# Kernel tuning notes

Hardware: AMD Instinct MI355X
Metric: run time of the kernel (lower is better)

Reference implementation:

```python
import jax, jax.numpy as jnp
import numpy as np

N, E = 100000, 1600000
NFEAT, NHID, NOUT, NHEADS = 512, 64, 64, 8
ALPHA = 0.2  # LeakyReLU negative slope


def setup_inputs() -> dict:
    key = jax.random.key(0)
    ks = jax.random.split(key, 12)
    feat = jax.random.normal(ks[0], (N, NFEAT), dtype=jnp.float32)
    edge_index = jax.random.randint(ks[1], (2, E), 0, N, dtype=jnp.int32)
    s = 0.05
    return {
        "feat": feat,
        "edge_index": edge_index,
        "fW_w": jax.random.normal(ks[2], (NHEADS, NHID, NFEAT), dtype=jnp.float32) * s,
        "fW_b": jnp.zeros((NHEADS, NHID), dtype=jnp.float32),
        "a_src": jax.random.normal(ks[3], (NHEADS, NHID), dtype=jnp.float32) * s,
        "a_dest": jax.random.normal(ks[4], (NHEADS, NHID), dtype=jnp.float32) * s,
        "W0": jax.random.normal(ks[5], (NHEADS, NHID, NFEAT), dtype=jnp.float32) * s,
        "b0": jnp.zeros((NHEADS, NHID), dtype=jnp.float32),
        "W1": jax.random.normal(ks[6], (NHEADS, NHID, NHEADS * NHID), dtype=jnp.float32) * s,
        "b1": jnp.zeros((NHEADS, NHID), dtype=jnp.float32),
        "lin_w": jax.random.normal(ks[7], (NOUT, NHEADS * NHID), dtype=jnp.float32) * s,
        "lin_b": jnp.zeros((NOUT,), dtype=jnp.float32),
    }


def reference(feat, edge_index, fW_w, fW_b, a_src, a_dest, W0, b0, W1, b1, lin_w, lin_b):
    n = feat.shape[0]
    row, col = edge_index[0], edge_index[1]

    # feature attention (all heads at once): h = fW(feat)  [N,H,D]
    h = jnp.einsum('nf,hdf->nhd', feat, fW_w) + fW_b
    f1 = jnp.einsum('nhd,hd->nh', h, a_src)   # [N,H]
    f2 = jnp.einsum('nhd,hd->nh', h, a_dest)  # [N,H]
    e = f1[row] + f2[col]                     # [E,H]
    e = jnp.where(e > 0, e, ALPHA * e)        # LeakyReLU
    # sparse softmax over each row's neighborhood (dim=1 of adj)
    m = jax.ops.segment_max(e, row, num_segments=n)    # [N,H]
    ex = jnp.exp(e - m[row])
    denom = jax.ops.segment_sum(ex, row, num_segments=n)
    attn = ex / denom[row]                    # [E,H]

    def spmm(vals, xw):  # vals [E], xw [N,D] -> [N,D]
        return jax.ops.segment_sum(vals[:, None] * xw[col], row, num_segments=n)

    x = feat
    for Wl, bl in ((W0, b0), (W1, b1)):
        outs = []
        for hidx in range(NHEADS):
            xw = x @ Wl[hidx].T + bl[hidx]           # [N,NHID]
            outs.append(jax.nn.elu(spmm(attn[:, hidx], xw)))
        x = jnp.concatenate(outs, axis=1)            # [N, H*NHID]

    return x @ lin_w.T + lin_b
```

## Files before the change

kernel.cpp:

```cpp
#include <hip/hip_runtime.h>
#include <hip/hip_bf16.h>
#include <math.h>

#define NFEAT 512
#define NHID  64
#define NHEADS 8
#define HD    512
#define NOUT  64

typedef _Float16 half8 __attribute__((ext_vector_type(8)));
typedef _Float16 half4 __attribute__((ext_vector_type(4)));
typedef float floatx4 __attribute__((ext_vector_type(4)));

__global__ void g_k(const float* __restrict__ fW_w, const float* __restrict__ fW_b,
                    const float* __restrict__ a_src, const float* __restrict__ a_dest,
                    float* __restrict__ G, float* __restrict__ C16)
{
    int idx = blockIdx.x * blockDim.x + threadIdx.x;
    if (idx < 16 * 512) {
        int r = idx >> 9;
        int f = idx & 511;
        int h = r & 7;
        const float* a = (r < 8) ? a_src : a_dest;
        float s = 0.f;
        #pragma unroll 8
        for (int d = 0; d < 64; ++d)
            s = fmaf(fW_w[(size_t)(h * 64 + d) * 512 + f], a[h * 64 + d], s);
        G[(size_t)r * 512 + f] = s;
    } else if (idx < 16 * 512 + 16) {
        int r = idx - 16 * 512;
        int h = r & 7;
        const float* a = (r < 8) ? a_src : a_dest;
        float s = 0.f;
        for (int d = 0; d < 64; ++d)
            s = fmaf(fW_b[h * 64 + d], a[h * 64 + d], s);
        C16[r] = s;
    }
}

#define FB_BM 128
#define FB_BK 64
__global__ __launch_bounds__(256) void f1f2_k(const float* __restrict__ feat,
    const float* __restrict__ G, const float* __restrict__ C16,
    float* __restrict__ f1, float* __restrict__ f2,
    _Float16* __restrict__ featH, int M)
{
    __shared__ float As[FB_BK][FB_BM + 4];
    __shared__ float Gs[16][FB_BK + 1];
    int tid = threadIdx.x;
    int tx = tid & 15;
    int ty = tid >> 4;
    int m0 = blockIdx.x * FB_BM;
    float acc[8] = {0.f, 0.f, 0.f, 0.f, 0.f, 0.f, 0.f, 0.f};

    for (int k0 = 0; k0 < NFEAT; k0 += FB_BK) {
        __syncthreads();
        #pragma unroll
        for (int j = 0; j < 8; ++j) {
            int fid = tid + 256 * j;
            int ml = fid >> 4;
            int k4 = fid & 15;
            float4 v = make_float4(0.f, 0.f, 0.f, 0.f);
            int gm = m0 + ml;
            if (gm < M) {
                v = *(const float4*)(feat + (size_t)gm * NFEAT + k0 + k4 * 4);
                half4 hv;
                hv[0] = (_Float16)v.x; hv[1] = (_Float16)v.y;
                hv[2] = (_Float16)v.z; hv[3] = (_Float16)v.w;
                *(half4*)(featH + (size_t)gm * NFEAT + k0 + k4 * 4) = hv;
            }
            As[k4 * 4 + 0][ml] = v.x;
            As[k4 * 4 + 1][ml] = v.y;
            As[k4 * 4 + 2][ml] = v.z;
            As[k4 * 4 + 3][ml] = v.w;
        }
        {
            int gr = tid >> 4;
            int k4 = tid & 15;
            float4 v = *(const float4*)(G + (size_t)gr * 512 + k0 + k4 * 4);
            Gs[gr][k4 * 4 + 0] = v.x;
            Gs[gr][k4 * 4 + 1] = v.y;
            Gs[gr][k4 * 4 + 2] = v.z;
            Gs[gr][k4 * 4 + 3] = v.w;
        }
        __syncthreads();
        #pragma unroll 16
        for (int kk = 0; kk < FB_BK; ++kk) {
            float g = Gs[tx][kk];
            #pragma unroll
            for (int i = 0; i < 8; ++i)
                acc[i] = fmaf(As[kk][ty + 16 * i], g, acc[i]);
        }
    }
    float c = C16[tx];
    #pragma unroll
    for (int i = 0; i < 8; ++i) {
        int gm = m0 + ty + 16 * i;
        if (gm < M) {
            float v = acc[i] + c;
            if (tx < 8) f1[(size_t)gm * 8 + tx] = v;
            else        f2[(size_t)gm * 8 + (tx - 8)] = v;
        }
    }
}

__global__ void zero_k(int* __restrict__ deg, int* __restrict__ fill, int n)
{
    int i = blockIdx.x * blockDim.x + threadIdx.x;
    if (i < n) { deg[i] = 0; fill[i] = 0; }
}

__global__ void count_k(const int* __restrict__ ei, int* __restrict__ deg, int E)
{
    int e = blockIdx.x * blockDim.x + threadIdx.x;
    if (e < E) atomicAdd(&deg[ei[e]], 1);
}

__global__ __launch_bounds__(1024) void bscan_k(const int* __restrict__ deg,
    int* __restrict__ row_ptr, int* __restrict__ bsum, int n)
{
    __shared__ int sh[1024];
    int tid = threadIdx.x;
    int i = blockIdx.x * 1024 + tid;
    int x = (i < n) ? deg[i] : 0;
    sh[tid] = x;
    __syncthreads();
    for (int off = 1; off < 1024; off <<= 1) {
        int v = (tid >= off) ? sh[tid - off] : 0;
        __syncthreads();
        sh[tid] += v;
        __syncthreads();
    }
    if (i < n) row_ptr[i] = sh[tid] - x;
    if (tid == 1023) bsum[blockIdx.x] = sh[1023];
}

__global__ void sscan_k(int* __restrict__ bsum, int nb)
{
    if (blockIdx.x == 0 && threadIdx.x == 0) {
        int run = 0;
        for (int b = 0; b < nb; ++b) { int t = bsum[b]; bsum[b] = run; run += t; }
    }
}

__global__ void addoff_k(int* __restrict__ row_ptr, const int* __restrict__ bsum,
                         int n, int Etot)
{
    int i = blockIdx.x * blockDim.x + threadIdx.x;
    if (i < n) row_ptr[i] += bsum[i >> 10];
    if (i == 0) row_ptr[n] = Etot;
}

__global__ void fill_k(const int* __restrict__ ei, const int* __restrict__ row_ptr,
                       int* __restrict__ fill, int* __restrict__ col_s, int E)
{
    int e = blockIdx.x * blockDim.x + threadIdx.x;
    if (e >= E) return;
    int r = ei[e];
    int c = ei[E + e];
    int o = atomicAdd(&fill[r], 1);
    col_s[row_ptr[r] + o] = c;
}

__global__ void attn_k(const int* __restrict__ row_ptr, const int* __restrict__ col_s,
                       const float* __restrict__ f1, const float* __restrict__ f2,
                       float* __restrict__ attn_s, float* __restrict__ inv_den,
                       int n_rows)
{
    int n = blockIdx.x * blockDim.x + threadIdx.x;
    if (n >= n_rows) return;
    int s = row_ptr[n], epos = row_ptr[n + 1];
    float4 fa = *(const float4*)(f1 + (size_t)n * 8);
    float4 fb = *(const float4*)(f1 + (size_t)n * 8 + 4);
    float F1[8] = {fa.x, fa.y, fa.z, fa.w, fb.x, fb.y, fb.z, fb.w};
    float den[8] = {0.f, 0.f, 0.f, 0.f, 0.f, 0.f, 0.f, 0.f};
    for (int p = s; p < epos; ++p) {
        int c = col_s[p];
        float4 ga = *(const float4*)(f2 + (size_t)c * 8);
        float4 gb = *(const float4*)(f2 + (size_t)c * 8 + 4);
        float F2[8] = {ga.x, ga.y, ga.z, ga.w, gb.x, gb.y, gb.z, gb.w};
        float ex[8];
        #pragma unroll
        for (int h = 0; h < 8; ++h) {
            float t = F1[h] + F2[h];
            t = (t > 0.f) ? t : 0.2f * t;
            ex[h] = expf(t);
            den[h] += ex[h];
        }
        float4* ap = (float4*)(attn_s + (size_t)p * 8);
        ap[0] = make_float4(ex[0], ex[1], ex[2], ex[3]);
        ap[1] = make_float4(ex[4], ex[5], ex[6], ex[7]);
    }
    float4* ip = (float4*)(inv_den + (size_t)n * 8);
    float iv[8];
    #pragma unroll
    for (int h = 0; h < 8; ++h) iv[h] = (den[h] > 0.f) ? 1.f / den[h] : 0.f;
    ip[0] = make_float4(iv[0], iv[1], iv[2], iv[3]);
    ip[1] = make_float4(iv[4], iv[5], iv[6], iv[7]);
}

__global__ void cvt_f16_k(const float* __restrict__ in, _Float16* __restrict__ out,
                          size_t n)
{
    size_t i = ((size_t)blockIdx.x * blockDim.x + threadIdx.x) * 8;
    if (i >= n) return;
    float4 a = *(const float4*)(in + i);
    float4 b = *(const float4*)(in + i + 4);
    half8 h;
    h[0] = (_Float16)a.x; h[1] = (_Float16)a.y; h[2] = (_Float16)a.z; h[3] = (_Float16)a.w;
    h[4] = (_Float16)b.x; h[5] = (_Float16)b.y; h[6] = (_Float16)b.z; h[7] = (_Float16)b.w;
    *(half8*)(out + i) = h;
}

#define TM 128
#define TN 128
#define TK 32
__global__ __launch_bounds__(256) void gemm_f16_mfma(
    const _Float16* __restrict__ A,
    const _Float16* __restrict__ B,
    const float* __restrict__ bias,
    _Float16* __restrict__ C,
    int M, int N, int K)
{
    __shared__ _Float16 smem_h[TM * TK + TN * TK];
    _Float16* Ash = smem_h;
    _Float16* Bsh = smem_h + TM * TK;
    int tid = threadIdx.x;
    int wave = tid >> 6;
    int lane = tid & 63;
    int m0 = blockIdx.x * TM;
    int n0 = blockIdx.y * TN;
    int wm = (wave & 1) * 64;
    int wn = (wave >> 1) * 64;

    floatx4 acc[4][4] = {};

    int fm = lane & 15;
    int q  = lane >> 4;

    for (int k0 = 0; k0 < K; k0 += TK) {
        __syncthreads();
        #pragma unroll
        for (int t = 0; t < 2; ++t) {
            int r = wave * 16 + t * 64;
            int gr = m0 + r + (lane >> 2);
            if (gr > M - 1) gr = M - 1;
            const _Float16* ga = A + (size_t)gr * K + k0 + (lane & 3) * 8;
            __builtin_amdgcn_global_load_lds(
                (const __attribute__((address_space(1))) void*)ga,
                (__attribute__((address_space(3))) void*)&Ash[r * TK], 16, 0, 0);
            const _Float16* gb = B + (size_t)(n0 + r + (lane >> 2)) * K + k0 + (lane & 3) * 8;
            __builtin_amdgcn_global_load_lds(
                (const __attribute__((address_space(1))) void*)gb,
                (__attribute__((address_space(3))) void*)&Bsh[r * TK], 16, 0, 0);
        }
        __syncthreads();
        half8 af[4], bf[4];
        #pragma unroll
        for (int i = 0; i < 4; ++i) {
            af[i] = *(const half8*)&Ash[(wm + i * 16 + fm) * TK + q * 8];
            bf[i] = *(const half8*)&Bsh[(wn + i * 16 + fm) * TK + q * 8];
        }
        #pragma unroll
        for (int i = 0; i < 4; ++i)
            #pragma unroll
            for (int j = 0; j < 4; ++j)
                acc[i][j] = __builtin_amdgcn_mfma_f32_16x16x32_f16(af[i], bf[j], acc[i][j], 0, 0, 0);
    }
    int cn = lane & 15;
    int rq = lane >> 4;
    _Float16* Csh = smem_h + wave * 1024;
    #pragma unroll
    for (int i = 0; i < 4; ++i) {
        __syncthreads();
        #pragma unroll
        for (int j = 0; j < 4; ++j) {
            int col = j * 16 + cn;
            float bsv = bias[n0 + wn + col];
            int scol = col ^ (rq * 16);
            #pragma unroll
            for (int r = 0; r < 4; ++r) {
                int row = rq * 4 + r;
                Csh[row * 64 + scol] = (_Float16)(acc[i][j][r] + bsv);
            }
        }
        __syncthreads();
        #pragma unroll
        for (int t = 0; t < 2; ++t) {
            int row = t * 8 + (lane >> 3);
            int c0 = (lane & 7) * 8;
            int sc0 = c0 ^ (((row >> 2) & 3) * 16);
            half8 v = *(const half8*)&Csh[row * 64 + sc0];
            int gm = m0 + wm + i * 16 + row;
            if (gm < M)
                *(half8*)&C[(size_t)gm * N + n0 + wn + c0] = v;
        }
    }
}

#define FG_TM 256
#define FG_TK 32
__global__ __launch_bounds__(256) void gemm_f16_n64(
    const _Float16* __restrict__ A,
    const _Float16* __restrict__ B,
    const float* __restrict__ bias,
    float* __restrict__ C,
    int M, int K)
{
    __shared__ _Float16 Ash[FG_TM * FG_TK];
    __shared__ _Float16 Bsh[64 * FG_TK];
    int tid = threadIdx.x;
    int wave = tid >> 6;
    int lane = tid & 63;
    int m0 = blockIdx.x * FG_TM;
    int wm = wave * 64;

    floatx4 acc[4][4] = {};
    int fm = lane & 15;
    int q  = lane >> 4;

    for (int k0 = 0; k0 < K; k0 += FG_TK) {
        __syncthreads();
        #pragma unroll
        for (int t = 0; t < 4; ++t) {
            int r = wave * 16 + t * 64;
            int gr = m0 + r + (lane >> 2);
            if (gr > M - 1) gr = M - 1;
            const _Float16* ga = A + (size_t)gr * K + k0 + (lane & 3) * 8;
            __builtin_amdgcn_global_load_lds(
                (const __attribute__((address_space(1))) void*)ga,
                (__attribute__((address_space(3))) void*)&Ash[r * FG_TK], 16, 0, 0);
        }
        {
            int r = wave * 16;
            const _Float16* gb = B + (size_t)(r + (lane >> 2)) * K + k0 + (lane & 3) * 8;
            __builtin_amdgcn_global_load_lds(
                (const __attribute__((address_space(1))) void*)gb,
                (__attribute__((address_space(3))) void*)&Bsh[r * FG_TK], 16, 0, 0);
        }
        __syncthreads();
        half8 af[4], bf[4];
        #pragma unroll
        for (int i = 0; i < 4; ++i) {
            af[i] = *(const half8*)&Ash[(wm + i * 16 + fm) * FG_TK + q * 8];
            bf[i] = *(const half8*)&Bsh[(i * 16 + fm) * FG_TK + q * 8];
        }
        #pragma unroll
        for (int i = 0; i < 4; ++i)
            #pragma unroll
            for (int j = 0; j < 4; ++j)
                acc[i][j] = __builtin_amdgcn_mfma_f32_16x16x32_f16(af[i], bf[j], acc[i][j], 0, 0, 0);
    }
    int cn = lane & 15;
    int rq = lane >> 4;
    #pragma unroll
    for (int i = 0; i < 4; ++i) {
        #pragma unroll
        for (int j = 0; j < 4; ++j) {
            int gn = j * 16 + cn;
            float bsv = bias[gn];
            #pragma unroll
            for (int r = 0; r < 4; ++r) {
                int gm = m0 + wm + i * 16 + rq * 4 + r;
                if (gm < M)
                    C[(size_t)gm * NOUT + gn] = acc[i][j][r] + bsv;
            }
        }
    }
}

__global__ __launch_bounds__(256) void agg_h_k(const int* __restrict__ row_ptr,
    const int* __restrict__ col_s, const float* __restrict__ attn_s,
    const float* __restrict__ inv_den, const _Float16* __restrict__ xw,
    _Float16* __restrict__ out, int n_rows)
{
    int wid = (blockIdx.x * blockDim.x + threadIdx.x) >> 6;
    int lane = threadIdx.x & 63;
    if (wid >= n_rows) return;
    int s = row_ptr[wid], e = row_ptr[wid + 1];
    int h = lane >> 3;
    float acc0[8] = {0.f, 0.f, 0.f, 0.f, 0.f, 0.f, 0.f, 0.f};
    float acc1[8] = {0.f, 0.f, 0.f, 0.f, 0.f, 0.f, 0.f, 0.f};
    float acc2[8] = {0.f, 0.f, 0.f, 0.f, 0.f, 0.f, 0.f, 0.f};
    float acc3[8] = {0.f, 0.f, 0.f, 0.f, 0.f, 0.f, 0.f, 0.f};
    int p = s;
    for (; p + 4 <= e; p += 4) {
        int c0 = col_s[p];
        int c1 = col_s[p + 1];
        int c2 = col_s[p + 2];
        int c3 = col_s[p + 3];
        float a0 = attn_s[(size_t)p * 8 + h];
        float a1 = attn_s[(size_t)(p + 1) * 8 + h];
        float a2 = attn_s[(size_t)(p + 2) * 8 + h];
        float a3 = attn_s[(size_t)(p + 3) * 8 + h];
        half8 x0 = *(const half8*)(xw + (size_t)c0 * HD + lane * 8);
        half8 x1 = *(const half8*)(xw + (size_t)c1 * HD + lane * 8);
        half8 x2 = *(const half8*)(xw + (size_t)c2 * HD + lane * 8);
        half8 x3 = *(const half8*)(xw + (size_t)c3 * HD + lane * 8);
        #pragma unroll
        for (int u = 0; u < 8; ++u) {
            acc0[u] = fmaf(a0, (float)x0[u], acc0[u]);
            acc1[u] = fmaf(a1, (float)x1[u], acc1[u]);
            acc2[u] = fmaf(a2, (float)x2[u], acc2[u]);
            acc3[u] = fmaf(a3, (float)x3[u], acc3[u]);
        }
    }
    for (; p < e; ++p) {
        int c0 = col_s[p];
        float a0 = attn_s[(size_t)p * 8 + h];
        half8 x0 = *(const half8*)(xw + (size_t)c0 * HD + lane * 8);
        #pragma unroll
        for (int u = 0; u < 8; ++u)
            acc0[u] = fmaf(a0, (float)x0[u], acc0[u]);
    }
    float inv = inv_den[(size_t)wid * 8 + h];
    half8 o;
    #pragma unroll
    for (int u = 0; u < 8; ++u) {
        float v = ((acc0[u] + acc1[u]) + (acc2[u] + acc3[u])) * inv;
        v = (v > 0.f) ? v : (expf(v) - 1.f);
        o[u] = (_Float16)v;
    }
    *(half8*)(out + (size_t)wid * HD + lane * 8) = o;
}

extern "C" void kernel_launch(void* const* d_in, const int* in_sizes, int n_in,
                              void* d_out, int out_size, void* d_ws, size_t ws_size,
                              hipStream_t stream)
{
    const float* feat   = (const float*)d_in[0];
    const int*   ei     = (const int*)  d_in[1];
    const float* fW_w   = (const float*)d_in[2];
    const float* fW_b   = (const float*)d_in[3];
    const float* a_src  = (const float*)d_in[4];
    const float* a_dest = (const float*)d_in[5];
    const float* W0     = (const float*)d_in[6];
    const float* b0     = (const float*)d_in[7];
    const float* W1     = (const float*)d_in[8];
    const float* b1     = (const float*)d_in[9];
    const float* lin_w  = (const float*)d_in[10];
    const float* lin_b  = (const float*)d_in[11];
    float* outp = (float*)d_out;

    const int N = in_sizes[0] / NFEAT;
    const int E = in_sizes[1] / 2;
    const int NB = (N + 1023) / 1024;

    char* ws = (char*)d_ws;
    size_t off = 0;
    auto carve = [&](size_t bytes) -> char* {
        char* p = ws + off;
        off += (bytes + 255) & ~(size_t)255;
        return p;
    };
    float*     G       = (float*)carve(16 * 512 * sizeof(float));
    float*     C16     = (float*)carve(16 * sizeof(float));
    float*     f1      = (float*)carve((size_t)N * 8 * sizeof(float));
    float*     f2      = (float*)carve((size_t)N * 8 * sizeof(float));
    int*       deg     = (int*)  carve((size_t)N * sizeof(int));
    int*       fillc   = (int*)  carve((size_t)N * sizeof(int));
    int*       row_ptr = (int*)  carve(((size_t)N + 1) * sizeof(int));
    int*       bsum    = (int*)  carve((size_t)NB * sizeof(int));
    int*       col_s   = (int*)  carve((size_t)E * sizeof(int));
    float*     attn_s  = (float*)carve((size_t)E * 8 * sizeof(float));
    float*     inv_den = (float*)carve((size_t)N * 8 * sizeof(float));
    _Float16*  W0h     = (_Float16*)carve((size_t)HD * NFEAT * sizeof(_Float16));
    _Float16*  W1h     = (_Float16*)carve((size_t)HD * HD * sizeof(_Float16));
    _Float16*  linWh   = (_Float16*)carve((size_t)NOUT * HD * sizeof(_Float16));
    _Float16*  hbuf1   = (_Float16*)carve((size_t)N * NFEAT * sizeof(_Float16));
    _Float16*  xwH     = (_Float16*)carve((size_t)N * HD * sizeof(_Float16));
    (void)ws_size; (void)n_in; (void)out_size;

    g_k<<<(16 * 512 + 16 + 255) / 256, 256, 0, stream>>>(fW_w, fW_b, a_src, a_dest, G, C16);
    f1f2_k<<<(N + FB_BM - 1) / FB_BM, 256, 0, stream>>>(feat, G, C16, f1, f2, hbuf1, N);
    zero_k<<<(N + 255) / 256, 256, 0, stream>>>(deg, fillc, N);
    count_k<<<(E + 255) / 256, 256, 0, stream>>>(ei, deg, E);
    bscan_k<<<NB, 1024, 0, stream>>>(deg, row_ptr, bsum, N);
    sscan_k<<<1, 64, 0, stream>>>(bsum, NB);
    addoff_k<<<(N + 255) / 256, 256, 0, stream>>>(row_ptr, bsum, N, E);
    fill_k<<<(E + 255) / 256, 256, 0, stream>>>(ei, row_ptr, fillc, col_s, E);
    attn_k<<<(N + 255) / 256, 256, 0, stream>>>(row_ptr, col_s, f1, f2, attn_s, inv_den, N);

    cvt_f16_k<<<(int)(((size_t)HD * NFEAT / 8 + 255) / 256), 256, 0, stream>>>(W0, W0h, (size_t)HD * NFEAT);
    cvt_f16_k<<<(int)(((size_t)HD * HD / 8 + 255) / 256), 256, 0, stream>>>(W1, W1h, (size_t)HD * HD);
    cvt_f16_k<<<(int)(((size_t)NOUT * HD / 8 + 255) / 256), 256, 0, stream>>>(lin_w, linWh, (size_t)NOUT * HD);

    gemm_f16_mfma<<<dim3((N + TM - 1) / TM, HD / TN), 256, 0, stream>>>(
        hbuf1, W0h, b0, xwH, N, HD, NFEAT);
    agg_h_k<<<((size_t)N * 64 + 255) / 256, 256, 0, stream>>>(
        row_ptr, col_s, attn_s, inv_den, xwH, hbuf1, N);
    gemm_f16_mfma<<<dim3((N + TM - 1) / TM, HD / TN), 256, 0, stream>>>(
        hbuf1, W1h, b1, xwH, N, HD, HD);
    agg_h_k<<<((size_t)N * 64 + 255) / 256, 256, 0, stream>>>(
        row_ptr, col_s, attn_s, inv_den, xwH, hbuf1, N);
    gemm_f16_n64<<<(N + FG_TM - 1) / FG_TM, 256, 0, stream>>>(
        hbuf1, linWh, lin_b, outp, N, HD);
}
```

Baseline: 1.298 ms.

## Parallelize attention per head, widen GEMM K tile with XOR swizzle, nontemporal aggregation

The attention kernel now uses one thread per (row, head) instead of one thread per row, giving eight times more parallelism, and it writes attention values with nontemporal stores. The MFMA GEMM doubles its K tile to 64, halving the number of barriers per K, and applies an XOR swizzle to the LDS layout to reduce bank conflicts. The aggregation kernel marks its col/attn stream loads and output stores as nontemporal so that the gathered xw rows stay in cache. The risks are more redundant col_s and f2 reads in the attention pass, a larger LDS footprint that may cut occupancy, and possible loss of L2 reuse of attn_s between the two aggregation passes.

```diff
diff --git a/kernel.cpp b/kernel.cpp
--- a/kernel.cpp
+++ b/kernel.cpp
@@ -167,36 +167,22 @@
                        float* __restrict__ attn_s, float* __restrict__ inv_den,
                        int n_rows)
 {
-    int n = blockIdx.x * blockDim.x + threadIdx.x;
+    int idx = blockIdx.x * blockDim.x + threadIdx.x;
+    int n = idx >> 3;
+    int h = idx & 7;
     if (n >= n_rows) return;
-    int s = row_ptr[n], epos = row_ptr[n + 1];
-    float4 fa = *(const float4*)(f1 + (size_t)n * 8);
-    float4 fb = *(const float4*)(f1 + (size_t)n * 8 + 4);
-    float F1[8] = {fa.x, fa.y, fa.z, fa.w, fb.x, fb.y, fb.z, fb.w};
-    float den[8] = {0.f, 0.f, 0.f, 0.f, 0.f, 0.f, 0.f, 0.f};
-    for (int p = s; p < epos; ++p) {
+    int s = row_ptr[n], e = row_ptr[n + 1];
+    float F1 = f1[(size_t)n * 8 + h];
+    float den = 0.f;
+    for (int p = s; p < e; ++p) {
         int c = col_s[p];
-        float4 ga = *(const float4*)(f2 + (size_t)c * 8);
-        float4 gb = *(const float4*)(f2 + (size_t)c * 8 + 4);
-        float F2[8] = {ga.x, ga.y, ga.z, ga.w, gb.x, gb.y, gb.z, gb.w};
-        float ex[8];
-        #pragma unroll
-        for (int h = 0; h < 8; ++h) {
-            float t = F1[h] + F2[h];
-            t = (t > 0.f) ? t : 0.2f * t;
-            ex[h] = expf(t);
-            den[h] += ex[h];
-        }
-        float4* ap = (float4*)(attn_s + (size_t)p * 8);
-        ap[0] = make_float4(ex[0], ex[1], ex[2], ex[3]);
-        ap[1] = make_float4(ex[4], ex[5], ex[6], ex[7]);
-    }
-    float4* ip = (float4*)(inv_den + (size_t)n * 8);
-    float iv[8];
-    #pragma unroll
-    for (int h = 0; h < 8; ++h) iv[h] = (den[h] > 0.f) ? 1.f / den[h] : 0.f;
-    ip[0] = make_float4(iv[0], iv[1], iv[2], iv[3]);
-    ip[1] = make_float4(iv[4], iv[5], iv[6], iv[7]);
+        float t = F1 + f2[(size_t)c * 8 + h];
+        t = (t > 0.f) ? t : 0.2f * t;
+        float ex = expf(t);
+        den += ex;
+        __builtin_nontemporal_store(ex, attn_s + (size_t)p * 8 + h);
+    }
+    inv_den[(size_t)n * 8 + h] = (den > 0.f) ? 1.f / den : 0.f;
 }
 
 __global__ void cvt_f16_k(const float* __restrict__ in, _Float16* __restrict__ out,
@@ -214,7 +200,7 @@
 
 #define TM 128
 #define TN 128
-#define TK 32
+#define TK 64
 __global__ __launch_bounds__(256) void gemm_f16_mfma(
     const _Float16* __restrict__ A,
     const _Float16* __restrict__ B,
@@ -237,35 +223,43 @@
 
     int fm = lane & 15;
     int q  = lane >> 4;
+    int lrow = lane >> 3;
+    int lcol = (lane & 7) ^ lrow;
 
     for (int k0 = 0; k0 < K; k0 += TK) {
         __syncthreads();
         #pragma unroll
-        for (int t = 0; t < 2; ++t) {
-            int r = wave * 16 + t * 64;
-            int gr = m0 + r + (lane >> 2);
+        for (int t = 0; t < 4; ++t) {
+            int r = wave * 8 + t * 32;
+            int gr = m0 + r + lrow;
             if (gr > M - 1) gr = M - 1;
-            const _Float16* ga = A + (size_t)gr * K + k0 + (lane & 3) * 8;
+            const _Float16* ga = A + (size_t)gr * K + k0 + lcol * 8;
             __builtin_amdgcn_global_load_lds(
                 (const __attribute__((address_space(1))) void*)ga,
                 (__attribute__((address_space(3))) void*)&Ash[r * TK], 16, 0, 0);
-            const _Float16* gb = B + (size_t)(n0 + r + (lane >> 2)) * K + k0 + (lane & 3) * 8;
+            const _Float16* gb = B + (size_t)(n0 + r + lrow) * K + k0 + lcol * 8;
             __builtin_amdgcn_global_load_lds(
                 (const __attribute__((address_space(1))) void*)gb,
                 (__attribute__((address_space(3))) void*)&Bsh[r * TK], 16, 0, 0);
         }
         __syncthreads();
-        half8 af[4], bf[4];
-        #pragma unroll
-        for (int i = 0; i < 4; ++i) {
-            af[i] = *(const half8*)&Ash[(wm + i * 16 + fm) * TK + q * 8];
-            bf[i] = *(const half8*)&Bsh[(wn + i * 16 + fm) * TK + q * 8];
-        }
-        #pragma unroll
-        for (int i = 0; i < 4; ++i)
-            #pragma unroll
-            for (int j = 0; j < 4; ++j)
-                acc[i][j] = __builtin_amdgcn_mfma_f32_16x16x32_f16(af[i], bf[j], acc[i][j], 0, 0, 0);
+        #pragma unroll
+        for (int kq = 0; kq < 2; ++kq) {
+            half8 af[4], bf[4];
+            int sw = ((kq << 2) + q);
+            #pragma unroll
+            for (int i = 0; i < 4; ++i) {
+                int ar = wm + i * 16 + fm;
+                af[i] = *(const half8*)&Ash[ar * TK + ((sw ^ (fm & 7)) << 3)];
+                int br = wn + i * 16 + fm;
+                bf[i] = *(const half8*)&Bsh[br * TK + ((sw ^ (fm & 7)) << 3)];
+            }
+            #pragma unroll
+            for (int i = 0; i < 4; ++i)
+                #pragma unroll
+                for (int j = 0; j < 4; ++j)
+                    acc[i][j] = __builtin_amdgcn_mfma_f32_16x16x32_f16(af[i], bf[j], acc[i][j], 0, 0, 0);
+        }
     }
     int cn = lane & 15;
     int rq = lane >> 4;
@@ -385,14 +379,14 @@
     float acc3[8] = {0.f, 0.f, 0.f, 0.f, 0.f, 0.f, 0.f, 0.f};
     int p = s;
     for (; p + 4 <= e; p += 4) {
-        int c0 = col_s[p];
-        int c1 = col_s[p + 1];
-        int c2 = col_s[p + 2];
-        int c3 = col_s[p + 3];
-        float a0 = attn_s[(size_t)p * 8 + h];
-        float a1 = attn_s[(size_t)(p + 1) * 8 + h];
-        float a2 = attn_s[(size_t)(p + 2) * 8 + h];
-        float a3 = attn_s[(size_t)(p + 3) * 8 + h];
+        int c0 = __builtin_nontemporal_load(col_s + p);
+        int c1 = __builtin_nontemporal_load(col_s + p + 1);
+        int c2 = __builtin_nontemporal_load(col_s + p + 2);
+        int c3 = __builtin_nontemporal_load(col_s + p + 3);
+        float a0 = __builtin_nontemporal_load(attn_s + (size_t)p * 8 + h);
+        float a1 = __builtin_nontemporal_load(attn_s + (size_t)(p + 1) * 8 + h);
+        float a2 = __builtin_nontemporal_load(attn_s + (size_t)(p + 2) * 8 + h);
+        float a3 = __builtin_nontemporal_load(attn_s + (size_t)(p + 3) * 8 + h);
         half8 x0 = *(const half8*)(xw + (size_t)c0 * HD + lane * 8);
         half8 x1 = *(const half8*)(xw + (size_t)c1 * HD + lane * 8);
         half8 x2 = *(const half8*)(xw + (size_t)c2 * HD + lane * 8);
@@ -406,8 +400,8 @@
         }
     }
     for (; p < e; ++p) {
-        int c0 = col_s[p];
-        float a0 = attn_s[(size_t)p * 8 + h];
+        int c0 = __builtin_nontemporal_load(col_s + p);
+        float a0 = __builtin_nontemporal_load(attn_s + (size_t)p * 8 + h);
         half8 x0 = *(const half8*)(xw + (size_t)c0 * HD + lane * 8);
         #pragma unroll
         for (int u = 0; u < 8; ++u)
@@ -421,7 +415,7 @@
         v = (v > 0.f) ? v : (expf(v) - 1.f);
         o[u] = (_Float16)v;
     }
-    *(half8*)(out + (size_t)wid * HD + lane * 8) = o;
+    __builtin_nontemporal_store(o, (half8*)(out + (size_t)wid * HD + lane * 8));
 }
 
 extern "C" void kernel_launch(void* const* d_in, const int* in_sizes, int n_in,
@@ -479,7 +473,7 @@
     sscan_k<<<1, 64, 0, stream>>>(bsum, NB);
     addoff_k<<<(N + 255) / 256, 256, 0, stream>>>(row_ptr, bsum, N, E);
     fill_k<<<(E + 255) / 256, 256, 0, stream>>>(ei, row_ptr, fillc, col_s, E);
-    attn_k<<<(N + 255) / 256, 256, 0, stream>>>(row_ptr, col_s, f1, f2, attn_s, inv_den, N);
+    attn_k<<<((size_t)N * 8 + 255) / 256, 256, 0, stream>>>(row_ptr, col_s, f1, f2, attn_s, inv_den, N);
 
     cvt_f16_k<<<(int)(((size_t)HD * NFEAT / 8 + 255) / 256), 256, 0, stream>>>(W0, W0h, (size_t)HD * NFEAT);
     cvt_f16_k<<<(int)(((size_t)HD * HD / 8 + 255) / 256), 256, 0, stream>>>(W1, W1h, (size_t)HD * HD);
```

New measurement: 1.327 ms. 1.02x slower.
